# Kernel optimization log

Hardware: AMD Instinct MI355X
Metric: run time of the kernel (lower is better)

Reference implementation:

```python
import jax, jax.numpy as jnp
import numpy as np

N = 20000       # nodes
E = 100000      # edges
STEPS = 4
ND = 128        # node feature dim
ED = 128        # edge feature dim
NIN = 128       # node input dim
EIN = 291       # edge input dim (2 + 17*17)
H = 64          # mpn edge-mlp hidden


def _lin(x, w, b):
    return x @ w + b


def setup_inputs():
    key = jax.random.key(0)
    ks = jax.random.split(key, 16)

    def w(k, i, o):
        return (jax.random.normal(k, (i, o), jnp.float32) / np.float32(np.sqrt(i)))

    d = {}
    d["x"] = jax.random.normal(ks[0], (N, NIN), jnp.float32)
    d["edge_attr"] = jax.random.normal(ks[1], (E, EIN), jnp.float32)
    d["edge_index"] = jax.random.randint(ks[2], (2, E), 0, N, jnp.int32)
    # node embedding MLP: NIN -> 128 -> ND (ReLU between, none after last)
    d["new0"] = w(ks[3], NIN, 128); d["neb0"] = jnp.zeros(128, jnp.float32)
    d["new1"] = w(ks[4], 128, ND); d["neb1"] = jnp.zeros(ND, jnp.float32)
    # edge embedding MLP: EIN -> 64 -> ED
    d["eew0"] = w(ks[5], EIN, 64); d["eeb0"] = jnp.zeros(64, jnp.float32)
    d["eew1"] = w(ks[6], 64, ED); d["eeb1"] = jnp.zeros(ED, jnp.float32)
    # MPN edge MLP (skip=True): 2*(2*ND) + 2*ED = 768 -> 64 -> ED, ReLU after each
    d["mew0"] = w(ks[7], 4 * ND + 2 * ED, H); d["meb0"] = jnp.zeros(H, jnp.float32)
    d["mew1"] = w(ks[8], H, ED); d["meb1"] = jnp.zeros(ED, jnp.float32)
    # MPN node MLP: 2*ND + ED = 384 -> ND, ReLU
    d["mnw0"] = w(ks[9], 2 * ND + ED, ND); d["mnb0"] = jnp.zeros(ND, jnp.float32)
    # classification MLP: ED -> 64 -> 32 -> 1
    d["cw0"] = w(ks[10], ED, 64); d["cb0"] = jnp.zeros(64, jnp.float32)
    d["cw1"] = w(ks[11], 64, 32); d["cb1"] = jnp.zeros(32, jnp.float32)
    d["cw2"] = w(ks[12], 32, 1); d["cb2"] = jnp.zeros(1, jnp.float32)
    return d


def reference(x, edge_attr, edge_index,
              new0, neb0, new1, neb1,
              eew0, eeb0, eew1, eeb1,
              mew0, meb0, mew1, meb1,
              mnw0, mnb0,
              cw0, cb0, cw1, cb1, cw2, cb2):
    relu = jax.nn.relu
    j, i = edge_index[0], edge_index[1]  # j: source, i: target

    nf = _lin(relu(_lin(x, new0, neb0)), new1, neb1)          # [N, ND]
    ef = _lin(relu(_lin(edge_attr, eew0, eeb0)), eew1, eeb1)  # [E, ED]
    nf0, ef0 = nf, ef

    for _ in range(STEPS):
        # skip connections: concat initial features
        nfc = jnp.concatenate([nf0, nf], axis=1)  # [N, 2*ND]
        efc = jnp.concatenate([ef0, ef], axis=1)  # [E, 2*ED]
        x_i = nfc[i]  # [E, 2*ND] target
        x_j = nfc[j]  # [E, 2*ND] source
        # edge update MLP (ReLU after both layers)
        h = relu(_lin(jnp.concatenate([x_i, x_j, efc], axis=1), mew0, meb0))
        ef = relu(_lin(h, mew1, meb1))  # [E, ED]
        # message: mlp_node([x_i, edge_attr_new]) aggregated at target i
        msg = relu(_lin(jnp.concatenate([x_i, ef], axis=1), mnw0, mnb0))  # [E, ND]
        nf = jax.ops.segment_sum(msg, i, num_segments=N)  # [N, ND]

    out = relu(_lin(ef, cw0, cb0))
    out = relu(_lin(out, cw1, cb1))
    out = _lin(out, cw2, cb2)  # [E, 1]
    return out
```

## Files before the change

### kernel.cpp

```cpp
#include <hip/hip_runtime.h>
#include <hip/hip_bf16.h>

#define ND 128
#define ED 128
#define NIN 128
#define EIN 291
#define KPAD 320
#define HH 64
#define TM 32
#define TS 64
#define GSE 768
#define MAXGE 3

typedef __attribute__((ext_vector_type(8))) short short8;
typedef __attribute__((ext_vector_type(4))) float float4_;

__device__ __forceinline__ unsigned short f2bf(float f)
{
    union { float f; unsigned u; } v; v.f = f;
    unsigned u = v.u;
    unsigned r = (u + 0x7FFFu + ((u >> 16) & 1u)) >> 16;
    return (unsigned short)r;
}
__device__ __forceinline__ float bf2f(unsigned short s)
{
    union { unsigned u; float f; } v; v.u = ((unsigned)s) << 16;
    return v.f;
}

template<int T, int KC, int K>
__device__ __forceinline__ void stage_frags(const unsigned short* __restrict__ src,
                                            unsigned short* __restrict__ wreg,
                                            int t, int k0)
{
    constexpr int TOT = T * KC * 64;
#pragma unroll
    for (int it = 0; it < TOT / 256; it++) {
        int idx = it * 256 + t;
        int f = idx >> 6, l = idx & 63;
        int col = (f / KC) * 16 + (l & 15);
        int k = (f % KC) * 32 + ((l >> 4) * 8);
        *(short8*)&wreg[idx * 8] = *(const short8*)&src[(size_t)col * K + k0 + k];
    }
}
#define FRAG(wreg, f, lane) (*(const short8*)&(wreg)[(((f) << 6) + (lane)) * 8])

__global__ __launch_bounds__(256) void zero_k(float* __restrict__ p, int n4)
{
    int idx = blockIdx.x * 256 + threadIdx.x;
    if (idx < n4) ((float4*)p)[idx] = make_float4(0.f, 0.f, 0.f, 0.f);
}

__global__ __launch_bounds__(256) void hist_k(const int* __restrict__ tgti,
                                              int* __restrict__ deg, int E)
{
    int e = blockIdx.x * 256 + threadIdx.x;
    if (e < E) atomicAdd(&deg[tgti[e]], 1);
}

__global__ __launch_bounds__(256) void scan_k(const int* __restrict__ deg,
                                              int* __restrict__ row_ptr,
                                              int* __restrict__ cursor, int N, int E)
{
    __shared__ int part[256];
    const int t = threadIdx.x;
    const int chunk = (N + 255) / 256;
    const int base = t * chunk;
    int s = 0;
    for (int k = 0; k < chunk; k++) { int idx = base + k; if (idx < N) s += deg[idx]; }
    part[t] = s;
    __syncthreads();
    for (int off = 1; off < 256; off <<= 1) {
        int v = (t >= off) ? part[t - off] : 0;
        __syncthreads();
        part[t] += v;
        __syncthreads();
    }
    int run = (t == 0) ? 0 : part[t - 1];
    for (int k = 0; k < chunk; k++) {
        int idx = base + k;
        if (idx < N) { row_ptr[idx] = run; cursor[idx] = run; run += deg[idx]; }
    }
    if (t == 255) row_ptr[N] = E;
}

__global__ __launch_bounds__(256) void scatter_k(const int* __restrict__ tgti,
                                                 int* __restrict__ cursor,
                                                 int* __restrict__ csr_eid, int E)
{
    int e = blockIdx.x * 256 + threadIdx.x;
    if (e < E) {
        int p = atomicAdd(&cursor[tgti[e]], 1);
        csr_eid[p] = e;
    }
}

__global__ __launch_bounds__(256) void agg_k(const int* __restrict__ row_ptr,
                                             const int* __restrict__ csr_eid,
                                             const unsigned short* __restrict__ msg,
                                             unsigned short* __restrict__ nf_bf, int N)
{
    int n = blockIdx.x * 2 + (threadIdx.x >> 7);
    int c = threadIdx.x & 127;
    if (n >= N) return;
    int beg = row_ptr[n], end = row_ptr[n + 1];
    float acc = 0.f;
    for (int k = beg; k < end; k++) {
        int e = csr_eid[k];
        acc += bf2f(msg[(size_t)e * ND + c]);
    }
    nf_bf[(size_t)n * ND + c] = f2bf(acc);
}

__global__ __launch_bounds__(256) void wprep_k(
    const float* __restrict__ mew0, const float* __restrict__ mew1, const float* __restrict__ mnw0,
    const float* __restrict__ eew0, const float* __restrict__ eew1, const float* __restrict__ cw0,
    const float* __restrict__ new0, const float* __restrict__ new1,
    unsigned short* __restrict__ w0T, unsigned short* __restrict__ w1T,
    unsigned short* __restrict__ wmT, unsigned short* __restrict__ w0eT,
    unsigned short* __restrict__ w1eT, unsigned short* __restrict__ cw0T,
    unsigned short* __restrict__ w0nT, unsigned short* __restrict__ w1nT)
{
    int idx = blockIdx.x * 256 + threadIdx.x;
    if (idx < 49152) {
        int c = idx / 768, k = idx % 768;
        w0T[idx] = f2bf(mew0[k * 64 + c]);
    } else if (idx < 57344) {
        int j = idx - 49152; int c = j / 64, k = j % 64;
        w1T[j] = f2bf(mew1[k * 128 + c]);
    } else if (idx < 106496) {
        int j = idx - 57344; int c = j / 384, k = j % 384;
        wmT[j] = f2bf(mnw0[k * 128 + c]);
    } else if (idx < 126976) {
        int j = idx - 106496; int c = j / KPAD, k = j % KPAD;
        w0eT[j] = (k < EIN) ? f2bf(eew0[k * 64 + c]) : (unsigned short)0;
    } else if (idx < 135168) {
        int j = idx - 126976; int c = j / 64, k = j % 64;
        w1eT[j] = f2bf(eew1[k * 128 + c]);
    } else if (idx < 143360) {
        int j = idx - 135168; int c = j / 128, k = j % 128;
        cw0T[j] = f2bf(cw0[k * 64 + c]);
    } else if (idx < 159744) {
        int j = idx - 143360; int c = j / 128, k = j % 128;
        w0nT[j] = f2bf(new0[k * 128 + c]);
    } else if (idx < 176128) {
        int j = idx - 159744; int c = j / 128, k = j % 128;
        w1nT[j] = f2bf(new1[k * 128 + c]);
    }
}

__global__ __launch_bounds__(256) void node_embed_k(
    const float* __restrict__ x,
    const unsigned short* __restrict__ w0nT, const float* __restrict__ b0,
    const unsigned short* __restrict__ w1nT, const float* __restrict__ b1,
    unsigned short* __restrict__ nf0_bf, unsigned short* __restrict__ nf_bf, int N)
{
    const int t = threadIdx.x;
    const int n0 = blockIdx.x * TM;
    __shared__ unsigned short wreg[8192];
    __shared__ unsigned short xin[TM][130];
    __shared__ unsigned short h_bf[TM][130];

#pragma unroll
    for (int it = 0; it < 4; it++) {
        int idx = it * 256 + t;
        int r = idx >> 5, c4 = idx & 31;
        int node = n0 + r; if (node >= N) node = N - 1;
        float4 v = *(const float4*)(x + (size_t)node * NIN + c4 * 4);
        unsigned lo = (unsigned)f2bf(v.x) | ((unsigned)f2bf(v.y) << 16);
        unsigned hi = (unsigned)f2bf(v.z) | ((unsigned)f2bf(v.w) << 16);
        *(uint2*)&xin[r][c4 * 4] = make_uint2(lo, hi);
    }

    const int w = t >> 6, lane = t & 63, quad = lane >> 4, n16 = lane & 15;
    const int m = w & 1, nh = w >> 1;

    float4_ acc[4];
#pragma unroll
    for (int q = 0; q < 4; q++) acc[q] = (float4_){0.f, 0.f, 0.f, 0.f};
#pragma unroll
    for (int hf = 0; hf < 2; hf++) {
        stage_frags<8, 2, 128>(w0nT, wreg, t, hf * 64);
        __syncthreads();
#pragma unroll
        for (int kc = 0; kc < 2; kc++) {
            short8 a = *(const short8*)&xin[m * 16 + n16][hf * 64 + kc * 32 + quad * 8];
#pragma unroll
            for (int tt = 0; tt < 4; tt++) {
                short8 b = FRAG(wreg, (nh * 4 + tt) * 2 + kc, lane);
                acc[tt] = __builtin_amdgcn_mfma_f32_16x16x32_bf16(a, b, acc[tt], 0, 0, 0);
            }
        }
        __syncthreads();
    }
#pragma unroll
    for (int tt = 0; tt < 4; tt++) {
        int c = nh * 64 + tt * 16 + n16;
        float bias = b0[c];
#pragma unroll
        for (int r4 = 0; r4 < 4; r4++)
            h_bf[m * 16 + quad * 4 + r4][c] = f2bf(fmaxf(acc[tt][r4] + bias, 0.f));
    }
    __syncthreads();

    float4_ acc2[4];
#pragma unroll
    for (int q = 0; q < 4; q++) acc2[q] = (float4_){0.f, 0.f, 0.f, 0.f};
#pragma unroll
    for (int hf = 0; hf < 2; hf++) {
        stage_frags<8, 2, 128>(w1nT, wreg, t, hf * 64);
        __syncthreads();
#pragma unroll
        for (int kc = 0; kc < 2; kc++) {
            short8 a = *(const short8*)&h_bf[m * 16 + n16][hf * 64 + kc * 32 + quad * 8];
#pragma unroll
            for (int tt = 0; tt < 4; tt++) {
                short8 b = FRAG(wreg, (nh * 4 + tt) * 2 + kc, lane);
                acc2[tt] = __builtin_amdgcn_mfma_f32_16x16x32_bf16(a, b, acc2[tt], 0, 0, 0);
            }
        }
        __syncthreads();
    }
#pragma unroll
    for (int tt = 0; tt < 4; tt++) {
        int c = nh * 64 + tt * 16 + n16;
        float bias = b1[c];
#pragma unroll
        for (int r4 = 0; r4 < 4; r4++) {
            int row = m * 16 + quad * 4 + r4;
            int node = n0 + row;
            if (node < N) {
                unsigned short v = f2bf(acc2[tt][r4] + bias);
                nf0_bf[(size_t)node * ND + c] = v;
                nf_bf[(size_t)node * ND + c] = v;
            }
        }
    }
}

__global__ __launch_bounds__(256, 3) void edge_embed_k(
    const float* __restrict__ ea,
    const unsigned short* __restrict__ w0eT, const float* __restrict__ b0,
    const unsigned short* __restrict__ w1eT, const float* __restrict__ b1,
    unsigned short* __restrict__ ef0_bf, unsigned short* __restrict__ ef_bf,
    int E, int ntiles)
{
    const int t = threadIdx.x;
    __shared__ unsigned short w0reg[10240];
    __shared__ unsigned short w1reg[8192];
    __shared__ unsigned short hsl[4][16 * 66];

    const int w = t >> 6, lane = t & 63, quad = lane >> 4, n16 = lane & 15;

    stage_frags<8, 2, 64>(w1eT, w1reg, t, 0);

    int ng = 0;
    int tile[MAXGE];
#pragma unroll
    for (int g = 0; g < MAXGE; g++) {
        int tl = blockIdx.x + g * GSE;
        if (tl < ntiles) { tile[g] = tl; ng = g + 1; }
        else tile[g] = 0;
    }

    float4_ accL[MAXGE][4];
#pragma unroll
    for (int g = 0; g < MAXGE; g++)
#pragma unroll
        for (int q = 0; q < 4; q++) accL[g][q] = (float4_){0.f, 0.f, 0.f, 0.f};

#pragma unroll
    for (int hf = 0; hf < 2; hf++) {
        __syncthreads();
        stage_frags<4, 5, KPAD>(w0eT, w0reg, t, hf * 160);
        __syncthreads();
#pragma unroll
        for (int g = 0; g < MAXGE; g++) {
            if (g < ng) {
                int e = tile[g] * 64 + w * 16 + n16; if (e >= E) e = E - 1;
                const float* src = ea + (size_t)e * EIN;
#pragma unroll
                for (int kc = 0; kc < 5; kc++) {
                    int k = hf * 160 + kc * 32 + quad * 8;
                    union { short8 s; uint4 u; } av;
                    if (k + 8 <= EIN) {
                        float4 v0 = *(const float4*)(src + k);
                        float4 v1 = *(const float4*)(src + k + 4);
                        av.u.x = (unsigned)f2bf(v0.x) | ((unsigned)f2bf(v0.y) << 16);
                        av.u.y = (unsigned)f2bf(v0.z) | ((unsigned)f2bf(v0.w) << 16);
                        av.u.z = (unsigned)f2bf(v1.x) | ((unsigned)f2bf(v1.y) << 16);
                        av.u.w = (unsigned)f2bf(v1.z) | ((unsigned)f2bf(v1.w) << 16);
                    } else {
                        unsigned short vv[8];
#pragma unroll
                        for (int j = 0; j < 8; j++)
                            vv[j] = (k + j < EIN) ? f2bf(src[k + j]) : (unsigned short)0;
                        av.u.x = (unsigned)vv[0] | ((unsigned)vv[1] << 16);
                        av.u.y = (unsigned)vv[2] | ((unsigned)vv[3] << 16);
                        av.u.z = (unsigned)vv[4] | ((unsigned)vv[5] << 16);
                        av.u.w = (unsigned)vv[6] | ((unsigned)vv[7] << 16);
                    }
#pragma unroll
                    for (int tt = 0; tt < 4; tt++) {
                        short8 b = FRAG(w0reg, tt * 5 + kc, lane);
                        accL[g][tt] = __builtin_amdgcn_mfma_f32_16x16x32_bf16(av.s, b, accL[g][tt], 0, 0, 0);
                    }
                }
            }
        }
    }

#pragma unroll
    for (int g = 0; g < MAXGE; g++) {
        if (g < ng) {
#pragma unroll
            for (int tt = 0; tt < 4; tt++) {
                int c = tt * 16 + n16;
                float bias = b0[c];
#pragma unroll
                for (int r4 = 0; r4 < 4; r4++)
                    hsl[w][(quad * 4 + r4) * 66 + c] = f2bf(fmaxf(accL[g][tt][r4] + bias, 0.f));
            }
            float4_ acc2[8];
#pragma unroll
            for (int q = 0; q < 8; q++) acc2[q] = (float4_){0.f, 0.f, 0.f, 0.f};
#pragma unroll
            for (int kc = 0; kc < 2; kc++) {
                short8 a2 = *(const short8*)&hsl[w][n16 * 66 + kc * 32 + quad * 8];
#pragma unroll
                for (int tt = 0; tt < 8; tt++)
                    acc2[tt] = __builtin_amdgcn_mfma_f32_16x16x32_bf16(
                        a2, FRAG(w1reg, tt * 2 + kc, lane), acc2[tt], 0, 0, 0);
            }
#pragma unroll
            for (int tt = 0; tt < 8; tt++) {
                int c = tt * 16 + n16;
                float bias = b1[c];
#pragma unroll
                for (int r4 = 0; r4 < 4; r4++) {
                    int e = tile[g] * 64 + w * 16 + quad * 4 + r4;
                    if (e < E) {
                        unsigned short v = f2bf(acc2[tt][r4] + bias);
                        ef0_bf[(size_t)e * ED + c] = v;
                        ef_bf[(size_t)e * ED + c] = v;
                    }
                }
            }
        }
    }
}

__global__ __launch_bounds__(256, 3) void edge_step_k(
    const int* __restrict__ srcj, const int* __restrict__ tgti,
    const unsigned short* __restrict__ nf0_bf, const unsigned short* __restrict__ nf_bf,
    const unsigned short* __restrict__ ef0_bf, unsigned short* __restrict__ ef_bf,
    unsigned short* __restrict__ msg,
    const unsigned short* __restrict__ w0T, const float* __restrict__ meb0,
    const unsigned short* __restrict__ w1T, const float* __restrict__ meb1,
    const unsigned short* __restrict__ wmT, const float* __restrict__ mnb0,
    int E, int wmsg)
{
    const int t = threadIdx.x;
    const int e0 = blockIdx.x * TS;
    __shared__ unsigned short wreg[8192];
    __shared__ unsigned short h_bf[TS][66];
    __shared__ unsigned short efn_bf[TS][130];

    const int w = t >> 6, lane = t & 63, quad = lane >> 4, n16 = lane & 15;
    const int erow = w * 16 + n16;
    int ec = e0 + erow; if (ec >= E) ec = E - 1;
    const int ti = tgti[ec], sj = srcj[ec];

    short8 areg[24];
    {
        const unsigned short* pAs[6] = {
            nf0_bf + (size_t)ti * ND + quad * 8,
            nf_bf  + (size_t)ti * ND + quad * 8,
            nf0_bf + (size_t)sj * ND + quad * 8,
            nf_bf  + (size_t)sj * ND + quad * 8,
            ef0_bf + (size_t)ec * ED + quad * 8,
            ef_bf  + (size_t)ec * ED + quad * 8 };
#pragma unroll
        for (int f = 0; f < 24; f++)
            areg[f] = *(const short8*)(pAs[f >> 2] + (f & 3) * 32);
    }

    float4_ accL[4];
#pragma unroll
    for (int q = 0; q < 4; q++) accL[q] = (float4_){0.f, 0.f, 0.f, 0.f};
#pragma unroll
    for (int hf = 0; hf < 6; hf++) {
        stage_frags<4, 4, 768>(w0T, wreg, t, hf * 128);
        __syncthreads();
#pragma unroll
        for (int kc = 0; kc < 4; kc++) {
#pragma unroll
            for (int tt = 0; tt < 4; tt++) {
                short8 b = FRAG(wreg, tt * 4 + kc, lane);
                accL[tt] = __builtin_amdgcn_mfma_f32_16x16x32_bf16(areg[hf * 4 + kc], b, accL[tt], 0, 0, 0);
            }
        }
        __syncthreads();
    }
#pragma unroll
    for (int tt = 0; tt < 4; tt++) {
        int c = tt * 16 + n16;
        float bias = meb0[c];
#pragma unroll
        for (int r4 = 0; r4 < 4; r4++)
            h_bf[w * 16 + quad * 4 + r4][c] = f2bf(fmaxf(accL[tt][r4] + bias, 0.f));
    }
    __syncthreads();

    stage_frags<8, 2, 64>(w1T, wreg, t, 0);
    __syncthreads();
    {
        float4_ acc[8];
#pragma unroll
        for (int q = 0; q < 8; q++) acc[q] = (float4_){0.f, 0.f, 0.f, 0.f};
#pragma unroll
        for (int kc = 0; kc < 2; kc++) {
            short8 a = *(const short8*)&h_bf[w * 16 + n16][kc * 32 + quad * 8];
#pragma unroll
            for (int tt = 0; tt < 8; tt++) {
                short8 b = FRAG(wreg, tt * 2 + kc, lane);
                acc[tt] = __builtin_amdgcn_mfma_f32_16x16x32_bf16(a, b, acc[tt], 0, 0, 0);
            }
        }
#pragma unroll
        for (int tt = 0; tt < 8; tt++) {
            int c = tt * 16 + n16;
            float bias = meb1[c];
#pragma unroll
            for (int r4 = 0; r4 < 4; r4++) {
                int row = w * 16 + quad * 4 + r4;
                unsigned short v = f2bf(fmaxf(acc[tt][r4] + bias, 0.f));
                efn_bf[row][c] = v;
                int e = e0 + row;
                if (e < E) ef_bf[(size_t)e * ED + c] = v;
            }
        }
    }
    __syncthreads();

    if (wmsg) {
        float4_ accM[8];
#pragma unroll
        for (int q = 0; q < 8; q++) accM[q] = (float4_){0.f, 0.f, 0.f, 0.f};
#pragma unroll
        for (int hf = 0; hf < 6; hf++) {
            stage_frags<8, 2, 384>(wmT, wreg, t, hf * 64);
            __syncthreads();
#pragma unroll
            for (int kc = 0; kc < 2; kc++) {
                int kk = hf * 2 + kc;
                short8 a;
                if (kk < 8) a = areg[kk];
                else        a = *(const short8*)&efn_bf[erow][(kk - 8) * 32 + quad * 8];
#pragma unroll
                for (int tt = 0; tt < 8; tt++) {
                    short8 b = FRAG(wreg, tt * 2 + kc, lane);
                    accM[tt] = __builtin_amdgcn_mfma_f32_16x16x32_bf16(a, b, accM[tt], 0, 0, 0);
                }
            }
            __syncthreads();
        }
#pragma unroll
        for (int tt = 0; tt < 8; tt++) {
            int c = tt * 16 + n16;
            float bias = mnb0[c];
#pragma unroll
            for (int r4 = 0; r4 < 4; r4++) {
                int row = w * 16 + quad * 4 + r4;
                int e = e0 + row;
                if (e < E)
                    msg[(size_t)e * ND + c] = f2bf(fmaxf(accM[tt][r4] + bias, 0.f));
            }
        }
    }
}

__global__ __launch_bounds__(256) void classify_k(
    const unsigned short* __restrict__ ef_bf,
    const unsigned short* __restrict__ cw0T, const float* __restrict__ cb0,
    const float* __restrict__ cw1, const float* __restrict__ cb1,
    const float* __restrict__ cw2, const float* __restrict__ cb2,
    float* __restrict__ out, int E)
{
    const int t = threadIdx.x;
    const int e0 = blockIdx.x * TM;
    __shared__ unsigned short h0_bf[TM][66];
    __shared__ float h1[TM][33];

    const int w = t >> 6, lane = t & 63, quad = lane >> 4, n16 = lane & 15;
    const int m = w & 1;
    const int erow = m * 16 + n16;
    int ec = e0 + erow; if (ec >= E) ec = E - 1;
    const unsigned short* pa = ef_bf + (size_t)ec * ED + quad * 8;

    {
        const int cb = (w >> 1) * 32;
        float4_ acc0 = {0.f, 0.f, 0.f, 0.f}, acc1 = acc0;
        const unsigned short* b0p = cw0T + (size_t)(cb + n16) * 128 + quad * 8;
        const unsigned short* b1p = b0p + (size_t)16 * 128;
#pragma unroll
        for (int kc = 0; kc < 4; kc++) {
            short8 a  = *(const short8*)(pa + kc * 32);
            short8 bb0 = *(const short8*)(b0p + kc * 32);
            short8 bb1 = *(const short8*)(b1p + kc * 32);
            acc0 = __builtin_amdgcn_mfma_f32_16x16x32_bf16(a, bb0, acc0, 0, 0, 0);
            acc1 = __builtin_amdgcn_mfma_f32_16x16x32_bf16(a, bb1, acc1, 0, 0, 0);
        }
#pragma unroll
        for (int t2 = 0; t2 < 2; t2++) {
            int c = cb + t2 * 16 + n16;
            float bias = cb0[c];
            float4_ ac = t2 ? acc1 : acc0;
#pragma unroll
            for (int r4 = 0; r4 < 4; r4++)
                h0_bf[m * 16 + quad * 4 + r4][c] = f2bf(fmaxf(ac[r4] + bias, 0.f));
        }
    }
    __syncthreads();

    {
        int c = t & 31;
        int rbase = (t >> 5) * 4;
#pragma unroll
        for (int q = 0; q < 4; q++) {
            int r = rbase + q;
            float acc = cb1[c];
#pragma unroll 8
            for (int k = 0; k < 64; k++) acc += bf2f(h0_bf[r][k]) * cw1[k * 32 + c];
            h1[r][c] = fmaxf(acc, 0.f);
        }
    }
    __syncthreads();

    if (t < TM) {
        int e = e0 + t;
        if (e < E) {
            float a = cb2[0];
#pragma unroll
            for (int k = 0; k < 32; k++) a += h1[t][k] * cw2[k];
            out[e] = a;
        }
    }
}

extern "C" void kernel_launch(void* const* d_in, const int* in_sizes, int n_in,
                              void* d_out, int out_size, void* d_ws, size_t ws_size,
                              hipStream_t stream)
{
    const float* x    = (const float*)d_in[0];
    const float* ea   = (const float*)d_in[1];
    const int*   eidx = (const int*)d_in[2];
    const float* new0 = (const float*)d_in[3];  const float* neb0 = (const float*)d_in[4];
    const float* new1 = (const float*)d_in[5];  const float* neb1 = (const float*)d_in[6];
    const float* eew0 = (const float*)d_in[7];  const float* eeb0 = (const float*)d_in[8];
    const float* eew1 = (const float*)d_in[9];  const float* eeb1 = (const float*)d_in[10];
    const float* mew0 = (const float*)d_in[11]; const float* meb0 = (const float*)d_in[12];
    const float* mew1 = (const float*)d_in[13]; const float* meb1 = (const float*)d_in[14];
    const float* mnw0 = (const float*)d_in[15]; const float* mnb0 = (const float*)d_in[16];
    const float* cw0  = (const float*)d_in[17]; const float* cb0  = (const float*)d_in[18];
    const float* cw1  = (const float*)d_in[19]; const float* cb1  = (const float*)d_in[20];
    const float* cw2  = (const float*)d_in[21]; const float* cb2  = (const float*)d_in[22];

    const int N = in_sizes[0] / NIN;
    const int E = in_sizes[2] / 2;
    const int* srcj = eidx;
    const int* tgti = eidx + E;

    char* wsb = (char*)d_ws;
    unsigned short* nf0_bf = (unsigned short*)wsb;
    unsigned short* nf_bf  = nf0_bf + (size_t)N * ND;
    unsigned short* ef0_bf = nf_bf + (size_t)N * ND;
    unsigned short* ef_bf  = ef0_bf + (size_t)E * ED;
    unsigned short* msg    = ef_bf + (size_t)E * ED;
    unsigned short* w0T  = msg + (size_t)E * ND;
    unsigned short* w1T  = w0T + 49152;
    unsigned short* wmT  = w1T + 8192;
    unsigned short* w0eT = wmT + 49152;
    unsigned short* w1eT = w0eT + 64 * KPAD;
    unsigned short* cw0T = w1eT + 8192;
    unsigned short* w0nT = cw0T + 8192;
    unsigned short* w1nT = w0nT + 16384;
    int* deg     = (int*)(w1nT + 16384);
    int* cursor  = deg + N;
    int* row_ptr = cursor + N;
    int* csr_eid = row_ptr + (N + 4);

    const int eblocks32 = (E + TM - 1) / TM;
    const int nblocks32 = (N + TM - 1) / TM;
    const int ntiles64 = (E + 63) / 64;

    wprep_k<<<(176128 + 255) / 256, 256, 0, stream>>>(mew0, mew1, mnw0, eew0, eew1, cw0,
                                                      new0, new1,
                                                      w0T, w1T, wmT, w0eT, w1eT, cw0T,
                                                      w0nT, w1nT);

    zero_k<<<((2 * N) / 4 + 255) / 256, 256, 0, stream>>>((float*)deg, (2 * N) / 4);
    hist_k<<<(E + 255) / 256, 256, 0, stream>>>(tgti, deg, E);
    scan_k<<<1, 256, 0, stream>>>(deg, row_ptr, cursor, N, E);
    scatter_k<<<(E + 255) / 256, 256, 0, stream>>>(tgti, cursor, csr_eid, E);

    node_embed_k<<<nblocks32, 256, 0, stream>>>(x, w0nT, neb0, w1nT, neb1,
                                                nf0_bf, nf_bf, N);
    edge_embed_k<<<GSE, 256, 0, stream>>>(ea, w0eT, eeb0, w1eT, eeb1,
                                          ef0_bf, ef_bf, E, ntiles64);

    for (int s = 0; s < 4; s++) {
        edge_step_k<<<ntiles64, 256, 0, stream>>>(srcj, tgti, nf0_bf, nf_bf,
                                                  ef0_bf, ef_bf, msg,
                                                  w0T, meb0, w1T, meb1, wmT, mnb0,
                                                  E, (s < 3) ? 1 : 0);
        if (s < 3)
            agg_k<<<(N + 1) / 2, 256, 0, stream>>>(row_ptr, csr_eid, msg, nf_bf, N);
    }

    classify_k<<<eblocks32, 256, 0, stream>>>(ef_bf, cw0T, cb0, cw1, cb1, cw2, cb2,
                                              (float*)d_out, E);
}
```

Baseline: 780.3 us.

## Stream A fragments per K-chunk and double weight staging chunk in edge step

Replaces the 24-register preload of all gathered A fragments with per-chunk loads, reloading the node features from global memory for the message GEMM. The weight staging buffer is doubled so each sync covers twice the K range, halving barrier count. The h and ef tiles now share one per-wave LDS buffer, and one barrier after the h write is dropped because each wave reads only its own rows. This lowers VGPR pressure at the cost of more LDS per block and repeated global gathers of x_i.

Result: faster. 760.1 us (-2.6%).

```diff
diff --git a/kernel.cpp b/kernel.cpp
--- a/kernel.cpp
+++ b/kernel.cpp
@@ -362,55 +362,51 @@
 {
     const int t = threadIdx.x;
     const int e0 = blockIdx.x * TS;
-    __shared__ unsigned short wreg[8192];
-    __shared__ unsigned short h_bf[TS][66];
-    __shared__ unsigned short efn_bf[TS][130];
+    __shared__ unsigned short wreg[16384];
+    __shared__ unsigned short hef[4][2080];
 
     const int w = t >> 6, lane = t & 63, quad = lane >> 4, n16 = lane & 15;
-    const int erow = w * 16 + n16;
-    int ec = e0 + erow; if (ec >= E) ec = E - 1;
+    int ec = e0 + w * 16 + n16; if (ec >= E) ec = E - 1;
     const int ti = tgti[ec], sj = srcj[ec];
 
-    short8 areg[24];
-    {
-        const unsigned short* pAs[6] = {
-            nf0_bf + (size_t)ti * ND + quad * 8,
-            nf_bf  + (size_t)ti * ND + quad * 8,
-            nf0_bf + (size_t)sj * ND + quad * 8,
-            nf_bf  + (size_t)sj * ND + quad * 8,
-            ef0_bf + (size_t)ec * ED + quad * 8,
-            ef_bf  + (size_t)ec * ED + quad * 8 };
-#pragma unroll
-        for (int f = 0; f < 24; f++)
-            areg[f] = *(const short8*)(pAs[f >> 2] + (f & 3) * 32);
-    }
+    const unsigned short* pAs[6] = {
+        nf0_bf + (size_t)ti * ND + quad * 8,
+        nf_bf  + (size_t)ti * ND + quad * 8,
+        nf0_bf + (size_t)sj * ND + quad * 8,
+        nf_bf  + (size_t)sj * ND + quad * 8,
+        ef0_bf + (size_t)ec * ED + quad * 8,
+        ef_bf  + (size_t)ec * ED + quad * 8 };
 
     float4_ accL[4];
 #pragma unroll
     for (int q = 0; q < 4; q++) accL[q] = (float4_){0.f, 0.f, 0.f, 0.f};
 #pragma unroll
-    for (int hf = 0; hf < 6; hf++) {
-        stage_frags<4, 4, 768>(w0T, wreg, t, hf * 128);
-        __syncthreads();
-#pragma unroll
-        for (int kc = 0; kc < 4; kc++) {
+    for (int hf = 0; hf < 3; hf++) {
+        short8 a8[8];
+#pragma unroll
+        for (int q2 = 0; q2 < 8; q2++)
+            a8[q2] = *(const short8*)(pAs[hf * 2 + (q2 >> 2)] + (q2 & 3) * 32);
+        stage_frags<4, 8, 768>(w0T, wreg, t, hf * 256);
+        __syncthreads();
+#pragma unroll
+        for (int kc = 0; kc < 8; kc++) {
 #pragma unroll
             for (int tt = 0; tt < 4; tt++) {
-                short8 b = FRAG(wreg, tt * 4 + kc, lane);
-                accL[tt] = __builtin_amdgcn_mfma_f32_16x16x32_bf16(areg[hf * 4 + kc], b, accL[tt], 0, 0, 0);
-            }
-        }
-        __syncthreads();
-    }
+                short8 b = FRAG(wreg, tt * 8 + kc, lane);
+                accL[tt] = __builtin_amdgcn_mfma_f32_16x16x32_bf16(a8[kc], b, accL[tt], 0, 0, 0);
+            }
+        }
+        __syncthreads();
+    }
+
 #pragma unroll
     for (int tt = 0; tt < 4; tt++) {
         int c = tt * 16 + n16;
         float bias = meb0[c];
 #pragma unroll
         for (int r4 = 0; r4 < 4; r4++)
-            h_bf[w * 16 + quad * 4 + r4][c] = f2bf(fmaxf(accL[tt][r4] + bias, 0.f));
-    }
-    __syncthreads();
+            hef[w][(quad * 4 + r4) * 66 + c] = f2bf(fmaxf(accL[tt][r4] + bias, 0.f));
+    }
 
     stage_frags<8, 2, 64>(w1T, wreg, t, 0);
     __syncthreads();
@@ -420,7 +416,7 @@
         for (int q = 0; q < 8; q++) acc[q] = (float4_){0.f, 0.f, 0.f, 0.f};
 #pragma unroll
         for (int kc = 0; kc < 2; kc++) {
-            short8 a = *(const short8*)&h_bf[w * 16 + n16][kc * 32 + quad * 8];
+            short8 a = *(const short8*)&hef[w][n16 * 66 + kc * 32 + quad * 8];
 #pragma unroll
             for (int tt = 0; tt < 8; tt++) {
                 short8 b = FRAG(wreg, tt * 2 + kc, lane);
@@ -433,10 +429,10 @@
             float bias = meb1[c];
 #pragma unroll
             for (int r4 = 0; r4 < 4; r4++) {
-                int row = w * 16 + quad * 4 + r4;
+                int row = quad * 4 + r4;
                 unsigned short v = f2bf(fmaxf(acc[tt][r4] + bias, 0.f));
-                efn_bf[row][c] = v;
-                int e = e0 + row;
+                hef[w][row * 130 + c] = v;
+                int e = e0 + w * 16 + row;
                 if (e < E) ef_bf[(size_t)e * ED + c] = v;
             }
         }
@@ -448,19 +444,25 @@
 #pragma unroll
         for (int q = 0; q < 8; q++) accM[q] = (float4_){0.f, 0.f, 0.f, 0.f};
 #pragma unroll
-        for (int hf = 0; hf < 6; hf++) {
-            stage_frags<8, 2, 384>(wmT, wreg, t, hf * 64);
+        for (int j = 0; j < 3; j++) {
+            short8 a4[4];
+            if (j < 2) {
+#pragma unroll
+                for (int q2 = 0; q2 < 4; q2++)
+                    a4[q2] = *(const short8*)(pAs[j] + q2 * 32);
+            } else {
+#pragma unroll
+                for (int q2 = 0; q2 < 4; q2++)
+                    a4[q2] = *(const short8*)&hef[w][n16 * 130 + q2 * 32 + quad * 8];
+            }
+            stage_frags<8, 4, 384>(wmT, wreg, t, j * 128);
             __syncthreads();
 #pragma unroll
-            for (int kc = 0; kc < 2; kc++) {
-                int kk = hf * 2 + kc;
-                short8 a;
-                if (kk < 8) a = areg[kk];
-                else        a = *(const short8*)&efn_bf[erow][(kk - 8) * 32 + quad * 8];
+            for (int kc = 0; kc < 4; kc++) {
 #pragma unroll
                 for (int tt = 0; tt < 8; tt++) {
-                    short8 b = FRAG(wreg, tt * 2 + kc, lane);
-                    accM[tt] = __builtin_amdgcn_mfma_f32_16x16x32_bf16(a, b, accM[tt], 0, 0, 0);
+                    short8 b = FRAG(wreg, tt * 4 + kc, lane);
+                    accM[tt] = __builtin_amdgcn_mfma_f32_16x16x32_bf16(a4[kc], b, accM[tt], 0, 0, 0);
                 }
             }
             __syncthreads();
```

## Process 128 edges per block in edge_step to reuse staged weight fragments

Applied to the files above, without the earlier changes.

The edge-step kernel now handles two 64-edge groups per block, so each staged weight chunk in shared memory feeds twice as many MFMAs. The 24-register preloaded A operands are replaced by per-chunk gathered loads issued just before each weight stage, and the message GEMM reloads node features from global memory instead of keeping them in registers. This halves the weight staging and barrier count per edge, but lowers the block count and adds repeated gathers of node features in the message phase.

Result: no change. 784.3 us (+0.5%).

```diff
diff --git a/kernel.cpp b/kernel.cpp
--- a/kernel.cpp
+++ b/kernel.cpp
@@ -8,7 +8,7 @@
 #define KPAD 320
 #define HH 64
 #define TM 32
-#define TS 64
+#define TS2 128
 #define GSE 768
 #define MAXGE 3
 
@@ -361,35 +361,44 @@
     int E, int wmsg)
 {
     const int t = threadIdx.x;
-    const int e0 = blockIdx.x * TS;
+    const int e0 = blockIdx.x * TS2;
     __shared__ unsigned short wreg[8192];
-    __shared__ unsigned short h_bf[TS][66];
-    __shared__ unsigned short efn_bf[TS][130];
+    __shared__ unsigned short hef[4][2][2080];
 
     const int w = t >> 6, lane = t & 63, quad = lane >> 4, n16 = lane & 15;
-    const int erow = w * 16 + n16;
-    int ec = e0 + erow; if (ec >= E) ec = E - 1;
-    const int ti = tgti[ec], sj = srcj[ec];
-
-    short8 areg[24];
-    {
-        const unsigned short* pAs[6] = {
-            nf0_bf + (size_t)ti * ND + quad * 8,
-            nf_bf  + (size_t)ti * ND + quad * 8,
-            nf0_bf + (size_t)sj * ND + quad * 8,
-            nf_bf  + (size_t)sj * ND + quad * 8,
-            ef0_bf + (size_t)ec * ED + quad * 8,
-            ef_bf  + (size_t)ec * ED + quad * 8 };
-#pragma unroll
-        for (int f = 0; f < 24; f++)
-            areg[f] = *(const short8*)(pAs[f >> 2] + (f & 3) * 32);
-    }
-
-    float4_ accL[4];
-#pragma unroll
-    for (int q = 0; q < 4; q++) accL[q] = (float4_){0.f, 0.f, 0.f, 0.f};
+
+    int ecg[2], tig[2], sjg[2];
+#pragma unroll
+    for (int g = 0; g < 2; g++) {
+        int e = e0 + g * 64 + w * 16 + n16;
+        if (e >= E) e = E - 1;
+        ecg[g] = e; tig[g] = tgti[e]; sjg[g] = srcj[e];
+    }
+
+    const unsigned short* pA[2][6];
+#pragma unroll
+    for (int g = 0; g < 2; g++) {
+        pA[g][0] = nf0_bf + (size_t)tig[g] * ND + quad * 8;
+        pA[g][1] = nf_bf  + (size_t)tig[g] * ND + quad * 8;
+        pA[g][2] = nf0_bf + (size_t)sjg[g] * ND + quad * 8;
+        pA[g][3] = nf_bf  + (size_t)sjg[g] * ND + quad * 8;
+        pA[g][4] = ef0_bf + (size_t)ecg[g] * ED + quad * 8;
+        pA[g][5] = ef_bf  + (size_t)ecg[g] * ED + quad * 8;
+    }
+
+    float4_ accL[2][4];
+#pragma unroll
+    for (int g = 0; g < 2; g++)
+#pragma unroll
+        for (int q = 0; q < 4; q++) accL[g][q] = (float4_){0.f, 0.f, 0.f, 0.f};
 #pragma unroll
     for (int hf = 0; hf < 6; hf++) {
+        short8 a[2][4];
+#pragma unroll
+        for (int g = 0; g < 2; g++)
+#pragma unroll
+            for (int q = 0; q < 4; q++)
+                a[g][q] = *(const short8*)(pA[g][hf] + q * 32);
         stage_frags<4, 4, 768>(w0T, wreg, t, hf * 128);
         __syncthreads();
 #pragma unroll
@@ -397,30 +406,34 @@
 #pragma unroll
             for (int tt = 0; tt < 4; tt++) {
                 short8 b = FRAG(wreg, tt * 4 + kc, lane);
-                accL[tt] = __builtin_amdgcn_mfma_f32_16x16x32_bf16(areg[hf * 4 + kc], b, accL[tt], 0, 0, 0);
-            }
-        }
-        __syncthreads();
-    }
-#pragma unroll
-    for (int tt = 0; tt < 4; tt++) {
-        int c = tt * 16 + n16;
-        float bias = meb0[c];
-#pragma unroll
-        for (int r4 = 0; r4 < 4; r4++)
-            h_bf[w * 16 + quad * 4 + r4][c] = f2bf(fmaxf(accL[tt][r4] + bias, 0.f));
-    }
-    __syncthreads();
+                accL[0][tt] = __builtin_amdgcn_mfma_f32_16x16x32_bf16(a[0][kc], b, accL[0][tt], 0, 0, 0);
+                accL[1][tt] = __builtin_amdgcn_mfma_f32_16x16x32_bf16(a[1][kc], b, accL[1][tt], 0, 0, 0);
+            }
+        }
+        __syncthreads();
+    }
+
+#pragma unroll
+    for (int g = 0; g < 2; g++)
+#pragma unroll
+        for (int tt = 0; tt < 4; tt++) {
+            int c = tt * 16 + n16;
+            float bias = meb0[c];
+#pragma unroll
+            for (int r4 = 0; r4 < 4; r4++)
+                hef[w][g][(quad * 4 + r4) * 66 + c] = f2bf(fmaxf(accL[g][tt][r4] + bias, 0.f));
+        }
 
     stage_frags<8, 2, 64>(w1T, wreg, t, 0);
     __syncthreads();
-    {
+#pragma unroll
+    for (int g = 0; g < 2; g++) {
         float4_ acc[8];
 #pragma unroll
         for (int q = 0; q < 8; q++) acc[q] = (float4_){0.f, 0.f, 0.f, 0.f};
 #pragma unroll
         for (int kc = 0; kc < 2; kc++) {
-            short8 a = *(const short8*)&h_bf[w * 16 + n16][kc * 32 + quad * 8];
+            short8 a = *(const short8*)&hef[w][g][n16 * 66 + kc * 32 + quad * 8];
 #pragma unroll
             for (int tt = 0; tt < 8; tt++) {
                 short8 b = FRAG(wreg, tt * 2 + kc, lane);
@@ -433,10 +446,10 @@
             float bias = meb1[c];
 #pragma unroll
             for (int r4 = 0; r4 < 4; r4++) {
-                int row = w * 16 + quad * 4 + r4;
+                int row = quad * 4 + r4;
                 unsigned short v = f2bf(fmaxf(acc[tt][r4] + bias, 0.f));
-                efn_bf[row][c] = v;
-                int e = e0 + row;
+                hef[w][g][row * 130 + c] = v;
+                int e = e0 + g * 64 + w * 16 + row;
                 if (e < E) ef_bf[(size_t)e * ED + c] = v;
             }
         }
@@ -444,39 +457,48 @@
     __syncthreads();
 
     if (wmsg) {
-        float4_ accM[8];
-#pragma unroll
-        for (int q = 0; q < 8; q++) accM[q] = (float4_){0.f, 0.f, 0.f, 0.f};
-#pragma unroll
-        for (int hf = 0; hf < 6; hf++) {
-            stage_frags<8, 2, 384>(wmT, wreg, t, hf * 64);
+        float4_ accM[2][8];
+#pragma unroll
+        for (int g = 0; g < 2; g++)
+#pragma unroll
+            for (int q = 0; q < 8; q++) accM[g][q] = (float4_){0.f, 0.f, 0.f, 0.f};
+#pragma unroll
+        for (int j = 0; j < 6; j++) {
+            short8 a[2][2];
+#pragma unroll
+            for (int g = 0; g < 2; g++)
+#pragma unroll
+                for (int kc = 0; kc < 2; kc++) {
+                    int kk = j * 2 + kc;
+                    if (kk < 8) a[g][kc] = *(const short8*)(pA[g][kk >> 2] + (kk & 3) * 32);
+                    else        a[g][kc] = *(const short8*)&hef[w][g][n16 * 130 + (kk - 8) * 32 + quad * 8];
+                }
+            stage_frags<8, 2, 384>(wmT, wreg, t, j * 64);
             __syncthreads();
 #pragma unroll
             for (int kc = 0; kc < 2; kc++) {
-                int kk = hf * 2 + kc;
-                short8 a;
-                if (kk < 8) a = areg[kk];
-                else        a = *(const short8*)&efn_bf[erow][(kk - 8) * 32 + quad * 8];
 #pragma unroll
                 for (int tt = 0; tt < 8; tt++) {
                     short8 b = FRAG(wreg, tt * 2 + kc, lane);
-                    accM[tt] = __builtin_amdgcn_mfma_f32_16x16x32_bf16(a, b, accM[tt], 0, 0, 0);
+                    accM[0][tt] = __builtin_amdgcn_mfma_f32_16x16x32_bf16(a[0][kc], b, accM[0][tt], 0, 0, 0);
+                    accM[1][tt] = __builtin_amdgcn_mfma_f32_16x16x32_bf16(a[1][kc], b, accM[1][tt], 0, 0, 0);
                 }
             }
             __syncthreads();
         }
 #pragma unroll
-        for (int tt = 0; tt < 8; tt++) {
-            int c = tt * 16 + n16;
-            float bias = mnb0[c];
-#pragma unroll
-            for (int r4 = 0; r4 < 4; r4++) {
-                int row = w * 16 + quad * 4 + r4;
-                int e = e0 + row;
-                if (e < E)
-                    msg[(size_t)e * ND + c] = f2bf(fmaxf(accM[tt][r4] + bias, 0.f));
-            }
-        }
+        for (int g = 0; g < 2; g++)
+#pragma unroll
+            for (int tt = 0; tt < 8; tt++) {
+                int c = tt * 16 + n16;
+                float bias = mnb0[c];
+#pragma unroll
+                for (int r4 = 0; r4 < 4; r4++) {
+                    int e = e0 + g * 64 + w * 16 + quad * 4 + r4;
+                    if (e < E)
+                        msg[(size_t)e * ND + c] = f2bf(fmaxf(accM[g][tt][r4] + bias, 0.f));
+                }
+            }
     }
 }
 
@@ -593,6 +615,7 @@
     const int eblocks32 = (E + TM - 1) / TM;
     const int nblocks32 = (N + TM - 1) / TM;
     const int ntiles64 = (E + 63) / 64;
+    const int ntiles128 = (E + TS2 - 1) / TS2;
 
     wprep_k<<<(176128 + 255) / 256, 256, 0, stream>>>(mew0, mew1, mnw0, eew0, eew1, cw0,
                                                       new0, new1,
@@ -610,10 +633,10 @@
                                           ef0_bf, ef_bf, E, ntiles64);
 
     for (int s = 0; s < 4; s++) {
-        edge_step_k<<<ntiles64, 256, 0, stream>>>(srcj, tgti, nf0_bf, nf_bf,
-                                                  ef0_bf, ef_bf, msg,
-                                                  w0T, meb0, w1T, meb1, wmT, mnb0,
-                                                  E, (s < 3) ? 1 : 0);
+        edge_step_k<<<ntiles128, 256, 0, stream>>>(srcj, tgti, nf0_bf, nf_bf,
+                                                   ef0_bf, ef_bf, msg,
+                                                   w0T, meb0, w1T, meb1, wmT, mnb0,
+                                                   E, (s < 3) ? 1 : 0);
         if (s < 3)
             agg_k<<<(N + 1) / 2, 256, 0, stream>>>(row_ptr, csr_eid, msg, nf_bf, N);
     }
```
